# Performance work log

Hardware: AMD Instinct MI355X
Metric: run time of the kernel (lower is better)

## Reference

```python
import jax, jax.numpy as jnp
import numpy as np

NUM_HEADS = 16
HEAD_DIM = 64  # latent_dim // num_heads = 1024 // 16


def setup_inputs() -> dict:
    key = jax.random.key(0)
    k1, k2, k3, k4 = jax.random.split(key, 4)
    B, S, C = 4, 2048, 1024
    x = jax.random.normal(k1, (B, S, C), dtype=jnp.float32)
    # torch nn.Linear weight layout: [out_features, in_features]
    W_qkv = jax.random.normal(k2, (2 * 1024 + C, C), dtype=jnp.float32) * (C ** -0.5)
    W_out = jax.random.normal(k3, (C, C), dtype=jnp.float32) * (C ** -0.5)
    b_out = jax.random.normal(k4, (C,), dtype=jnp.float32) * 0.01
    return {"x": x, "W_qkv": W_qkv, "W_out": W_out, "b_out": b_out}


def reference(x, W_qkv, W_out, b_out):
    B, S, C = x.shape
    H, CH = NUM_HEADS, HEAD_DIM
    qkv = jnp.einsum('bsc,oc->bso', x, W_qkv)          # [B, S, 2*latent + C]
    qkv = qkv.reshape(B, S, H, -1)                      # per-head: [CH, CH, C//H]
    q = qkv[..., :CH]
    k = qkv[..., CH:2 * CH]
    v = qkv[..., 2 * CH:]
    energy = jnp.einsum('bqhc,bkhc->bhqk', q, k)        # full score matrix
    scale = jnp.asarray(C, x.dtype) ** 0.5              # note: original scales by sqrt(C), not sqrt(head_dim)
    attn = jax.nn.softmax(energy / scale, axis=-1)
    out = jnp.einsum('bhqk,bkhc->bqhc', attn, v).reshape(B, S, -1)
    out = jnp.einsum('bsc,oc->bso', out, W_out) + b_out
    return out + x
```

## Files before the change

### kernel.cpp

```cpp
#include <hip/hip_runtime.h>
#include <hip/hip_bf16.h>
#include <stdint.h>

#define BB 4
#define SS 2048
#define CC 1024
#define HH 16
#define DD 64
#define MTOT (BB*SS)
#define NQKV 3072

typedef __attribute__((ext_vector_type(8))) short short8;
typedef __attribute__((ext_vector_type(4))) float f32x4;
typedef __attribute__((ext_vector_type(16))) float f32x16;
typedef __attribute__((ext_vector_type(4))) unsigned uint4v;
typedef __attribute__((ext_vector_type(2))) unsigned uint2v;

#define MFMA16(A,B,C) __builtin_amdgcn_mfma_f32_16x16x32_bf16((A),(B),(C),0,0,0)
#define MFMA32(A,B,C) __builtin_amdgcn_mfma_f32_32x32x16_bf16((A),(B),(C),0,0,0)
#define BARRIER() asm volatile("s_barrier" ::: "memory")

__device__ __forceinline__ ushort f2bf(float f) {
  uint32_t u = __builtin_bit_cast(uint32_t, f);
  u += 0x7FFFu + ((u >> 16) & 1u);
  return (ushort)(u >> 16);
}

__device__ __forceinline__ float bf2f(ushort u) {
  return __builtin_bit_cast(float, (uint32_t)u << 16);
}

__device__ __forceinline__ unsigned cvtpk(float lo, float hi) {
  unsigned r;
  asm("v_cvt_pk_bf16_f32 %0, %1, %2" : "=v"(r) : "v"(lo), "v"(hi));
  return r;
}

__device__ __forceinline__ float hw_exp2(float x) {
  float r;
  asm("v_exp_f32 %0, %1" : "=v"(r) : "v"(x));
  return r;
}

__device__ __forceinline__ f32x16 zero16() {
  f32x16 v;
  #pragma unroll
  for (int i = 0; i < 16; ++i) v[i] = 0.f;
  return v;
}

__global__ void cvt3_kernel(const float* __restrict__ a, ushort* __restrict__ da, int na4,
                            const float* __restrict__ b, ushort* __restrict__ db, int nb4,
                            const float* __restrict__ c, ushort* __restrict__ dc, int nc4) {
  int total = na4 + nb4 + nc4;
  int stride = gridDim.x * blockDim.x;
  for (int i = blockIdx.x * blockDim.x + threadIdx.x; i < total; i += stride) {
    const float4* s; ushort4* d; int k;
    if (i < na4)            { s = (const float4*)a; d = (ushort4*)da; k = i; }
    else if (i < na4 + nb4) { s = (const float4*)b; d = (ushort4*)db; k = i - na4; }
    else                    { s = (const float4*)c; d = (ushort4*)dc; k = i - na4 - nb4; }
    float4 v = s[k];
    ushort4 o;
    o.x = f2bf(v.x); o.y = f2bf(v.y); o.z = f2bf(v.z); o.w = f2bf(v.w);
    d[k] = o;
  }
}

__device__ __forceinline__ void stage_half128(const ushort* __restrict__ gsrc, ushort* ldsbase, int tid) {
  #pragma unroll
  for (int ld = 0; ld < 4; ++ld) {
    int ci = ld * 256 + tid;
    int row = ci >> 3, slot = ci & 7;
    const ushort* src = gsrc + (size_t)row * 1024 + ((slot ^ (row & 7)) << 3);
    __builtin_amdgcn_global_load_lds(
        (const __attribute__((address_space(1))) uint32_t*)src,
        (__attribute__((address_space(3))) uint32_t*)(ldsbase + ci * 8), 16, 0, 0);
  }
}

__device__ __forceinline__ short8 rd_frag(const ushort* Lb, int row, int slot) {
  return *(const short8*)(Lb + row * 64 + ((slot ^ (row & 7)) << 3));
}

__device__ __forceinline__ void core128(const ushort* __restrict__ A, const ushort* __restrict__ Bw,
                                        int m0, int n0, ushort* L, f32x4 acc[4][4]) {
  const int tid = threadIdx.x, lane = tid & 63, w = tid >> 6;
  const int q = lane & 15, g = lane >> 4;
  const int wm = (w >> 1) * 64, wn = (w & 1) * 64;
  const ushort* Ag = A + (size_t)m0 * 1024;
  const ushort* Bg = Bw + (size_t)n0 * 1024;

  #pragma unroll
  for (int tt = 0; tt < 2; ++tt) {
    stage_half128(Ag + tt * 64, L + tt * 16384, tid);
    stage_half128(Bg + tt * 64, L + tt * 16384 + 8192, tid);
  }
  asm volatile("s_waitcnt vmcnt(8)" ::: "memory");
  BARRIER();

  #pragma unroll 1
  for (int t = 0; t < 16; ++t) {
    const ushort* La = L + (t & 1) * 16384;
    const ushort* Lb = La + 8192;
    short8 af[4][2], bf[4][2];
    #pragma unroll
    for (int mi = 0; mi < 4; ++mi)
      #pragma unroll
      for (int ks = 0; ks < 2; ++ks)
        af[mi][ks] = rd_frag(La, wm + mi * 16 + q, ks * 4 + g);
    #pragma unroll
    for (int nj = 0; nj < 4; ++nj)
      #pragma unroll
      for (int ks = 0; ks < 2; ++ks)
        bf[nj][ks] = rd_frag(Lb, wn + nj * 16 + q, ks * 4 + g);
    #pragma unroll
    for (int mi = 0; mi < 4; ++mi)
      #pragma unroll
      for (int nj = 0; nj < 4; ++nj) {
        acc[mi][nj] = MFMA16(af[mi][0], bf[nj][0], acc[mi][nj]);
        acc[mi][nj] = MFMA16(af[mi][1], bf[nj][1], acc[mi][nj]);
      }
    BARRIER();
    if (t <= 13) {
      ushort* Ls = L + (t & 1) * 16384;
      stage_half128(Ag + (t + 2) * 64, Ls, tid);
      stage_half128(Bg + (t + 2) * 64, Ls + 8192, tid);
      asm volatile("s_waitcnt vmcnt(8)" ::: "memory");
      BARRIER();
    } else if (t == 14) {
      asm volatile("s_waitcnt vmcnt(0)" ::: "memory");
      BARRIER();
    }
  }
}

__global__ __launch_bounds__(256, 2) void gemm_qkv(const ushort* __restrict__ xb, const ushort* __restrict__ wqkv,
                                                   ushort* __restrict__ qfbuf, ushort* __restrict__ kfbuf,
                                                   ushort* __restrict__ vfbuf) {
  __shared__ __align__(16) ushort L[32768];
  const int bid = blockIdx.x;
  const int xcd = bid & 7, r0 = bid >> 3;
  const int m0 = (r0 / 3) * 128, n0 = (xcd * 3 + (r0 % 3)) * 128;

  f32x4 acc[4][4];
  #pragma unroll
  for (int i = 0; i < 4; ++i)
    #pragma unroll
    for (int j = 0; j < 4; ++j) acc[i][j] = f32x4{0.f, 0.f, 0.f, 0.f};
  core128(xb, wqkv, m0, n0, L, acc);

  const int lane = threadIdx.x & 63, wave = threadIdx.x >> 6;
  const int g = lane >> 4, q = lane & 15;
  const int wm = (wave >> 1) * 64, wn = (wave & 1) * 64;
  const int s0 = m0 & 2047, bb = m0 >> 11;

  #pragma unroll
  for (int j = 0; j < 4; ++j) {
    int n = n0 + wn + j * 16 + q;
    int h = n / 192;
    int which = (n - h * 192) >> 6;
    float scl = (which == 0) ? 0.045084222f : 1.0f;
    int nc = wn + j * 16 + q;
    #pragma unroll
    for (int i = 0; i < 4; ++i) {
      #pragma unroll
      for (int rr = 0; rr < 4; ++rr) {
        int mr = wm + i * 16 + g * 4 + rr;
        L[mr * 128 + (nc ^ ((mr & 7) << 4))] = f2bf(acc[i][j][rr] * scl);
      }
    }
  }
  __syncthreads();

  {
    const int n_g = n0 + wave * 32;
    const int h = n_g / 192, rem = n_g - h * 192, which = rem >> 6;
    const int bh = bb * 16 + h;
    if (which < 2) {
      ushort* dst0 = (which == 0) ? qfbuf : kfbuf;
      const int c0 = (rem & 63) >> 5;
      #pragma unroll
      for (int k = 0; k < 8; ++k) {
        int jt = (s0 >> 4) + k;
        int mr = k * 16 + (lane & 15);
        int nc0 = wave * 32 + (lane >> 4) * 8;
        short8 v = *(const short8*)(L + mr * 128 + (nc0 ^ ((mr & 7) << 4)));
        *(short8*)(dst0 + ((((size_t)bh * 128 + jt) * 2 + c0) * 64 + lane) * 8) = v;
      }
    } else {
      const int ct0 = (rem & 63) >> 4;
      #pragma unroll
      for (int k = 0; k < 8; ++k) {
        int jcr = k >> 1, ct = ct0 + (k & 1);
        int nc = wave * 32 + (k & 1) * 16 + (lane & 15);
        int mrb = jcr * 32 + (lane >> 4) * 8;
        short8 v;
        #pragma unroll
        for (int e = 0; e < 8; ++e) {
          int mr = mrb + e;
          v[e] = (short)L[mr * 128 + (nc ^ ((mr & 7) << 4))];
        }
        int jc = (s0 >> 5) + jcr;
        *(short8*)(vfbuf + ((((size_t)bh * 64 + jc) * 4 + ct) * 64 + lane) * 8) = v;
      }
    }
  }
}

__global__ __launch_bounds__(256, 2) void gemm_out(const ushort* __restrict__ ab, const ushort* __restrict__ wout,
                                                   const ushort* __restrict__ xbb, const float* __restrict__ bias,
                                                   float* __restrict__ out) {
  __shared__ __align__(16) ushort L[32768];
  const int bid = blockIdx.x;
  const int sw = (bid & 7) * 64 + (bid >> 3);
  const int m0 = (sw & 63) * 128, n0 = (sw >> 6) * 128;

  f32x4 acc[4][4];
  #pragma unroll
  for (int i = 0; i < 4; ++i)
    #pragma unroll
    for (int j = 0; j < 4; ++j) acc[i][j] = f32x4{0.f, 0.f, 0.f, 0.f};
  core128(ab, wout, m0, n0, L, acc);

  const int tid = threadIdx.x;
  const int lane = tid & 63, wave = tid >> 6;
  const int g = lane >> 4, q = lane & 15;
  const int wm = (wave >> 1) * 64, wn = (wave & 1) * 64;
  float* Lf = reinterpret_cast<float*>(L);

  #pragma unroll
  for (int j = 0; j < 4; ++j) {
    int nc = wn + j * 16 + q;
    #pragma unroll
    for (int i = 0; i < 4; ++i) {
      #pragma unroll
      for (int rr = 0; rr < 4; ++rr) {
        int mr = wm + i * 16 + g * 4 + rr;
        int swz = ((mr & 4) << 0) | ((mr & 8) << 1);
        Lf[mr * 128 + (nc ^ swz)] = acc[i][j][rr];
      }
    }
  }
  __syncthreads();

  #pragma unroll
  for (int k = 0; k < 16; ++k) {
    int ci = k * 256 + tid;
    int row = ci >> 5, cb = (ci & 31) * 4;
    int swz = ((row & 4) << 0) | ((row & 8) << 1);
    float4 v = *(const float4*)(Lf + row * 128 + (cb ^ swz));
    size_t m = (size_t)(m0 + row);
    int n = n0 + cb;
    ushort4 xr = *(const ushort4*)(xbb + m * 1024 + n);
    float4 bv = *(const float4*)(bias + n);
    float4 o;
    o.x = v.x + bv.x + bf2f(xr.x);
    o.y = v.y + bv.y + bf2f(xr.y);
    o.z = v.z + bv.z + bf2f(xr.z);
    o.w = v.w + bv.w + bf2f(xr.w);
    *(float4*)(out + m * 1024 + n) = o;
  }
}

__device__ __forceinline__ void attn_step32(const short8 kf[4], const short8 vf[2][2],
                                            const short8 qf[4], const short8 onesf,
                                            f32x16& oa0, f32x16& oa1, f32x16& la, int hi) {
  f32x16 sa = zero16();
  __builtin_amdgcn_s_setprio(1);
  #pragma unroll
  for (int kc = 0; kc < 4; ++kc) sa = MFMA32(kf[kc], qf[kc], sa);
  __builtin_amdgcn_s_setprio(0);

  unsigned w[8];
  #pragma unroll
  for (int i = 0; i < 8; ++i)
    w[i] = cvtpk(hw_exp2(sa[2 * i]), hw_exp2(sa[2 * i + 1]));

  #pragma unroll
  for (int kj = 0; kj < 2; ++kj) {
    uint2v p0 = __builtin_amdgcn_permlane32_swap(w[kj * 4 + 2], w[kj * 4 + 0], false, false);
    uint2v p1 = __builtin_amdgcn_permlane32_swap(w[kj * 4 + 3], w[kj * 4 + 1], false, false);
    uint4v t;
    t.x = p0[1];
    t.y = p1[1];
    t.z = p0[0];
    t.w = p1[0];
    short8 pa = __builtin_bit_cast(short8, t);
    __builtin_amdgcn_s_setprio(1);
    oa0 = MFMA32(pa, vf[kj][0], oa0);
    oa1 = MFMA32(pa, vf[kj][1], oa1);
    la  = MFMA32(pa, onesf, la);
    __builtin_amdgcn_s_setprio(0);
  }
}

__global__ __launch_bounds__(256) void attn_kernel(const ushort* __restrict__ QF, const ushort* __restrict__ KF,
                                                   const ushort* __restrict__ VF, ushort* __restrict__ aout) {
  const int bid = blockIdx.x;
  const int xcd = bid & 7, r = bid >> 3;
  const int qb = r & 15, bh = xcd + (r >> 4) * 8;
  const int lane = threadIdx.x & 63, wave = threadIdx.x >> 6;
  const int l31 = lane & 31, hi = lane >> 5, l15 = lane & 15, l31h = l31 >> 4;
  const int qt = qb * 4 + wave;

  const ushort* QFb = QF + (size_t)bh * 131072;
  const ushort* KFb = KF + (size_t)bh * 131072;
  const ushort* VFb = VF + (size_t)bh * 131072;

  short8 onesf;
  #pragma unroll
  for (int e = 0; e < 8; ++e) onesf[e] = (short)0x3F80;

  short8 qf[4];
  #pragma unroll
  for (int kc = 0; kc < 4; ++kc) {
    int jt16 = qt * 2 + l31h;
    int lane2 = (((kc * 2 + hi) & 3) << 4) + l15;
    qf[kc] = *(const short8*)(QFb + ((size_t)(jt16 * 2 + (kc >> 1)) * 64 + lane2) * 8);
  }

  f32x16 oa0 = zero16(), oa1 = zero16(), la = zero16();

  short8 kfA[4], kfB[4], vfA[2][2], vfB[2][2];
  #pragma unroll
  for (int kc = 0; kc < 4; ++kc) {
    int lane2 = (((kc * 2 + hi) & 3) << 4) + l15;
    kfA[kc] = *(const short8*)(KFb + ((size_t)(l31h * 2 + (kc >> 1)) * 64 + lane2) * 8);
  }

  #pragma unroll 1
  for (int j0 = 0; j0 < SS; j0 += 64) {
    #pragma unroll
    for (int kj = 0; kj < 2; ++kj)
      #pragma unroll
      for (int cb = 0; cb < 2; ++cb) {
        int ct = cb * 2 + l31h;
        int lane16 = (((kj * 2 + hi) & 3) << 4) + l15;
        vfA[kj][cb] = *(const short8*)(VFb + ((size_t)((j0 >> 5) * 4 + ct) * 64 + lane16) * 8);
      }
    #pragma unroll
    for (int kc = 0; kc < 4; ++kc) {
      int jt16 = ((j0 + 32) >> 4) + l31h;
      int lane2 = (((kc * 2 + hi) & 3) << 4) + l15;
      kfB[kc] = *(const short8*)(KFb + ((size_t)(jt16 * 2 + (kc >> 1)) * 64 + lane2) * 8);
    }

    attn_step32(kfA, vfA, qf, onesf, oa0, oa1, la, hi);

    #pragma unroll
    for (int kj = 0; kj < 2; ++kj)
      #pragma unroll
      for (int cb = 0; cb < 2; ++cb) {
        int ct = cb * 2 + l31h;
        int lane16 = (((kj * 2 + hi) & 3) << 4) + l15;
        vfB[kj][cb] = *(const short8*)(VFb + ((size_t)(((j0 + 32) >> 5) * 4 + ct) * 64 + lane16) * 8);
      }
    if (j0 + 64 < SS) {
      #pragma unroll
      for (int kc = 0; kc < 4; ++kc) {
        int jt16 = ((j0 + 64) >> 4) + l31h;
        int lane2 = (((kc * 2 + hi) & 3) << 4) + l15;
        kfA[kc] = *(const short8*)(KFb + ((size_t)(jt16 * 2 + (kc >> 1)) * 64 + lane2) * 8);
      }
    }

    attn_step32(kfB, vfB, qf, onesf, oa0, oa1, la, hi);
  }

  const int b = bh >> 4, h = bh & 15;
  #pragma unroll
  for (int r16 = 0; r16 < 16; ++r16) {
    float inv = 1.0f / la[r16];
    int row = qt * 32 + (r16 & 3) + 8 * (r16 >> 2) + 4 * hi;
    size_t base = ((size_t)b * SS + row) * CC + h * DD;
    aout[base + l31]      = f2bf(oa0[r16] * inv);
    aout[base + 32 + l31] = f2bf(oa1[r16] * inv);
  }
}

extern "C" void kernel_launch(void* const* d_in, const int* in_sizes, int n_in,
                              void* d_out, int out_size, void* d_ws, size_t ws_size,
                              hipStream_t stream) {
  const float* x    = (const float*)d_in[0];
  const float* wqkv = (const float*)d_in[1];
  const float* wout = (const float*)d_in[2];
  const float* bias = (const float*)d_in[3];
  float* out = (float*)d_out;

  ushort* xb    = (ushort*)d_ws;
  ushort* wqkvb = xb + (size_t)8 * 1024 * 1024;
  ushort* woutb = wqkvb + (size_t)3 * 1024 * 1024;
  ushort* qfbuf = woutb + (size_t)1024 * 1024;
  ushort* kfbuf = qfbuf + (size_t)8 * 1024 * 1024;
  ushort* vfbuf = kfbuf + (size_t)8 * 1024 * 1024;
  ushort* aout  = vfbuf + (size_t)8 * 1024 * 1024;

  hipLaunchKernelGGL(cvt3_kernel, dim3(2048), dim3(256), 0, stream,
                     x, xb, 8 * 1024 * 1024 / 4,
                     wqkv, wqkvb, 3 * 1024 * 1024 / 4,
                     wout, woutb, 1024 * 1024 / 4);

  hipLaunchKernelGGL(gemm_qkv, dim3(1536), dim3(256), 0, stream,
                     xb, wqkvb, qfbuf, kfbuf, vfbuf);
  hipLaunchKernelGGL(attn_kernel, dim3(1024), dim3(256), 0, stream,
                     qfbuf, kfbuf, vfbuf, aout);
  hipLaunchKernelGGL(gemm_out, dim3(512), dim3(256), 0, stream,
                     aout, woutb, xb, bias, out);
}
```

Before: 200.2 us.

## Process two query tiles per wave in attention to reuse K/V fragments

Each attention wave now handles two 32-row query tiles instead of one. Every K and V fragment loaded from global memory feeds both tiles, which halves K/V load traffic per unit of work and interleaves two independent QK/exp/PV chains for more instruction-level parallelism. The grid shrinks from 1024 to 512 blocks. In exchange the kernel uses roughly double the accumulator registers, which can lower occupancy or cause spills, and the smaller grid gives fewer waves for latency hiding.

After: 201.6 us. Within noise of the previous version (+0.7%).

```diff
diff --git a/kernel.cpp b/kernel.cpp
--- a/kernel.cpp
+++ b/kernel.cpp
@@ -262,29 +262,27 @@
   }
 }
 
-__device__ __forceinline__ void attn_step32(const short8 kf[4], const short8 vf[2][2],
-                                            const short8 qf[4], const short8 onesf,
-                                            f32x16& oa0, f32x16& oa1, f32x16& la, int hi) {
+__device__ __forceinline__ f32x16 qk32(const short8 kf[4], const short8 qf[4]) {
   f32x16 sa = zero16();
   __builtin_amdgcn_s_setprio(1);
   #pragma unroll
   for (int kc = 0; kc < 4; ++kc) sa = MFMA32(kf[kc], qf[kc], sa);
   __builtin_amdgcn_s_setprio(0);
-
+  return sa;
+}
+
+__device__ __forceinline__ void exppv32(const f32x16& sa, const short8 vf[2][2],
+                                        const short8 onesf, f32x16& oa0, f32x16& oa1, f32x16& la) {
   unsigned w[8];
   #pragma unroll
   for (int i = 0; i < 8; ++i)
     w[i] = cvtpk(hw_exp2(sa[2 * i]), hw_exp2(sa[2 * i + 1]));
-
   #pragma unroll
   for (int kj = 0; kj < 2; ++kj) {
     uint2v p0 = __builtin_amdgcn_permlane32_swap(w[kj * 4 + 2], w[kj * 4 + 0], false, false);
     uint2v p1 = __builtin_amdgcn_permlane32_swap(w[kj * 4 + 3], w[kj * 4 + 1], false, false);
     uint4v t;
-    t.x = p0[1];
-    t.y = p1[1];
-    t.z = p0[0];
-    t.w = p1[0];
+    t.x = p0[1]; t.y = p1[1]; t.z = p0[0]; t.w = p1[0];
     short8 pa = __builtin_bit_cast(short8, t);
     __builtin_amdgcn_s_setprio(1);
     oa0 = MFMA32(pa, vf[kj][0], oa0);
@@ -298,10 +296,10 @@
                                                    const ushort* __restrict__ VF, ushort* __restrict__ aout) {
   const int bid = blockIdx.x;
   const int xcd = bid & 7, r = bid >> 3;
-  const int qb = r & 15, bh = xcd + (r >> 4) * 8;
+  const int qb = r & 7, bh = xcd + (r >> 3) * 8;
   const int lane = threadIdx.x & 63, wave = threadIdx.x >> 6;
   const int l31 = lane & 31, hi = lane >> 5, l15 = lane & 15, l31h = l31 >> 4;
-  const int qt = qb * 4 + wave;
+  const int qt0 = qb * 8 + wave * 2;
 
   const ushort* QFb = QF + (size_t)bh * 131072;
   const ushort* KFb = KF + (size_t)bh * 131072;
@@ -311,15 +309,18 @@
   #pragma unroll
   for (int e = 0; e < 8; ++e) onesf[e] = (short)0x3F80;
 
-  short8 qf[4];
-  #pragma unroll
-  for (int kc = 0; kc < 4; ++kc) {
-    int jt16 = qt * 2 + l31h;
-    int lane2 = (((kc * 2 + hi) & 3) << 4) + l15;
-    qf[kc] = *(const short8*)(QFb + ((size_t)(jt16 * 2 + (kc >> 1)) * 64 + lane2) * 8);
-  }
-
-  f32x16 oa0 = zero16(), oa1 = zero16(), la = zero16();
+  short8 qf[2][4];
+  #pragma unroll
+  for (int t = 0; t < 2; ++t)
+    #pragma unroll
+    for (int kc = 0; kc < 4; ++kc) {
+      int jt16 = (qt0 + t) * 2 + l31h;
+      int lane2 = (((kc * 2 + hi) & 3) << 4) + l15;
+      qf[t][kc] = *(const short8*)(QFb + ((size_t)(jt16 * 2 + (kc >> 1)) * 64 + lane2) * 8);
+    }
+
+  f32x16 oa00 = zero16(), oa01 = zero16(), la0 = zero16();
+  f32x16 oa10 = zero16(), oa11 = zero16(), la1 = zero16();
 
   short8 kfA[4], kfB[4], vfA[2][2], vfB[2][2];
   #pragma unroll
@@ -345,7 +346,12 @@
       kfB[kc] = *(const short8*)(KFb + ((size_t)(jt16 * 2 + (kc >> 1)) * 64 + lane2) * 8);
     }
 
-    attn_step32(kfA, vfA, qf, onesf, oa0, oa1, la, hi);
+    {
+      f32x16 sa0 = qk32(kfA, qf[0]);
+      f32x16 sa1 = qk32(kfA, qf[1]);
+      exppv32(sa0, vfA, onesf, oa00, oa01, la0);
+      exppv32(sa1, vfA, onesf, oa10, oa11, la1);
+    }
 
     #pragma unroll
     for (int kj = 0; kj < 2; ++kj)
@@ -364,17 +370,30 @@
       }
     }
 
-    attn_step32(kfB, vfB, qf, onesf, oa0, oa1, la, hi);
+    {
+      f32x16 sa0 = qk32(kfB, qf[0]);
+      f32x16 sa1 = qk32(kfB, qf[1]);
+      exppv32(sa0, vfB, onesf, oa00, oa01, la0);
+      exppv32(sa1, vfB, onesf, oa10, oa11, la1);
+    }
   }
 
   const int b = bh >> 4, h = bh & 15;
   #pragma unroll
   for (int r16 = 0; r16 < 16; ++r16) {
-    float inv = 1.0f / la[r16];
-    int row = qt * 32 + (r16 & 3) + 8 * (r16 >> 2) + 4 * hi;
-    size_t base = ((size_t)b * SS + row) * CC + h * DD;
-    aout[base + l31]      = f2bf(oa0[r16] * inv);
-    aout[base + 32 + l31] = f2bf(oa1[r16] * inv);
+    int rowoff = (r16 & 3) + 8 * (r16 >> 2) + 4 * hi;
+    {
+      float inv = 1.0f / la0[r16];
+      size_t base = ((size_t)b * SS + qt0 * 32 + rowoff) * CC + h * DD;
+      aout[base + l31]      = f2bf(oa00[r16] * inv);
+      aout[base + 32 + l31] = f2bf(oa01[r16] * inv);
+    }
+    {
+      float inv = 1.0f / la1[r16];
+      size_t base = ((size_t)b * SS + (qt0 + 1) * 32 + rowoff) * CC + h * DD;
+      aout[base + l31]      = f2bf(oa10[r16] * inv);
+      aout[base + 32 + l31] = f2bf(oa11[r16] * inv);
+    }
   }
 }
 
@@ -402,7 +421,7 @@
 
   hipLaunchKernelGGL(gemm_qkv, dim3(1536), dim3(256), 0, stream,
                      xb, wqkvb, qfbuf, kfbuf, vfbuf);
-  hipLaunchKernelGGL(attn_kernel, dim3(1024), dim3(256), 0, stream,
+  hipLaunchKernelGGL(attn_kernel, dim3(512), dim3(256), 0, stream,
                      qfbuf, kfbuf, vfbuf, aout);
   hipLaunchKernelGGL(gemm_out, dim3(512), dim3(256), 0, stream,
                      aout, woutb, xb, bias, out);
```
